# Optimization experiments

Measured on AMD Instinct MI355X. Metric: run time of the kernel, lower is better.

The kernel has to match this reference:

```python
import jax, jax.numpy as jnp
import numpy as np

IN_FEAT = 3 * 299 * 299  # 268203
D1 = 512
H = 28
OUT = 2


def setup_inputs() -> dict:
    key = jax.random.key(0)
    ks = jax.random.split(key, 10)
    B, T = 4, 64
    s1 = 1.0 / np.sqrt(IN_FEAT)
    s2 = 1.0 / np.sqrt(D1)
    s3 = 1.0 / np.sqrt(H)
    return {
        "x": jax.random.normal(ks[0], (B, T, 3, 299, 299), jnp.float32),
        "W1": jax.random.uniform(ks[1], (IN_FEAT, D1), jnp.float32, -s1, s1),
        "b1": jax.random.uniform(ks[2], (D1,), jnp.float32, -s1, s1),
        "Wi": jax.random.uniform(ks[3], (D1, H), jnp.float32, -s2, s2),
        "Wr": jax.random.uniform(ks[4], (H, H), jnp.float32, -s3, s3),
        "br": jax.random.uniform(ks[5], (H,), jnp.float32, -s3, s3),
        "A": jax.random.normal(ks[6], (H,), jnp.float32),
        "tau": 1.0 + jax.random.uniform(ks[7], (H,), jnp.float32),  # positive time constants
        "W2": jax.random.uniform(ks[8], (H, OUT), jnp.float32, -s3, s3),
        "b2": jax.random.uniform(ks[9], (OUT,), jnp.float32, -s3, s3),
    }


def reference(x, W1, b1, Wi, Wr, br, A, tau, W2, b2):
    B, T = x.shape[0], x.shape[1]
    xf = x.reshape(B, T, -1)                      # [B, T, 268203]
    h1 = jax.nn.relu(jnp.einsum('btf,fd->btd', xf, W1) + b1)  # [B, T, 512]
    u = jnp.einsum('btd,dh->bth', h1, Wi)         # precomputed input drive [B, T, H]
    dt = 1.0

    def step(h, u_t):
        # fused-Euler LTC cell: f gates both time-constant and attractor A
        ft = jax.nn.sigmoid(u_t + h @ Wr + br)
        h_new = (h + dt * ft * A) / (1.0 + dt * (1.0 / tau + ft))
        return h_new, h_new

    h0 = jnp.zeros((B, H), x.dtype)
    _, hs = jax.lax.scan(step, h0, jnp.swapaxes(u, 0, 1))  # [T, B, H]
    last = jax.nn.relu(hs[-1])                    # relu then take last step
    out = last @ W2 + b2                          # [B, 2]
    return jax.nn.sigmoid(out)
```

## Files before the change

### kernel.cpp

```cpp
#include <hip/hip_runtime.h>
#include <hip/hip_bf16.h>

#define KTOT   268203
#define MROWS  256
#define NCOLS  512
#define HDIM   28
#define NSTEPS 8382
#define FSTEP  8381
#define KREM   11
#define BN     256

typedef __attribute__((ext_vector_type(4))) float  f32x4;
typedef __attribute__((ext_vector_type(8))) __bf16 bf16x8;

#define AUX_NT 2

static __device__ inline bf16x8 pack8(const float* f) {
    union { bf16x8 v; __hip_bfloat16 h[8]; } u;
    #pragma unroll
    for (int j = 0; j < 8; ++j) u.h[j] = __float2bfloat16(f[j]);
    return u.v;
}
static __device__ inline unsigned short bfbits(float v) {
    __hip_bfloat16 h = __float2bfloat16(v);
    union { __hip_bfloat16 h; unsigned short u; } c; c.h = h; return c.u;
}

__global__ __launch_bounds__(512, 2) void gemm1_kernel(
    const float* __restrict__ x, const float* __restrict__ W1,
    __hip_bfloat16* __restrict__ part, int steps_per, int nks)
{
    __shared__ __align__(16) float Albuf[2][MROWS * 32];
    __shared__ __align__(16) float Bbuf[2][32 * BN];

    const int tid  = threadIdx.x;
    const int lane = tid & 63;
    const int w    = tid >> 6;
    const int wm   = w >> 1;
    const int wn   = w & 1;

    int bx, ks;
    {
        const int id = blockIdx.x;
        if ((nks & 7) == 0) {
            const int xcd = id & 7;
            const int m_  = id >> 3;
            bx = m_ & 1;
            ks = ((m_ >> 1) << 3) | xcd;
        } else {
            bx = id & 1;
            ks = id >> 1;
        }
    }
    const int bcol = bx * BN;

    const int dlt = lane >> 5;
    const int m   = lane & 31;
    const int rw7 = (2 * w + dlt) & 7;
    const int ag  = (m >> 2) ^ rw7;
    const size_t a_off = (size_t)(2 * w + dlt) * KTOT + ag * 4 + (m & 3);
    const size_t b_off = bcol + (size_t)(lane) * 4;

    f32x4 acc[4][8];
    #pragma unroll
    for (int i = 0; i < 4; ++i)
        #pragma unroll
        for (int j = 0; j < 8; ++j)
            acc[i][j] = (f32x4){0.f, 0.f, 0.f, 0.f};

    const int s0 = ks * steps_per;
    int s1 = s0 + steps_per;
    if (s1 > NSTEPS) s1 = NSTEPS;
    int s1f = (s1 < FSTEP) ? s1 : FSTEP;
    int nfull = s1f - s0;
    if (nfull < 0) nfull = 0;

    auto issue_step = [&](int s, int buf) {
        const float* ap = x + a_off + (size_t)s * 32;
        #pragma unroll
        for (int i = 0; i < 16; ++i) {
            const float* gp = ap + (size_t)i * 16 * KTOT;
            char* lp = (char*)&Albuf[buf][0] + (i * 8 + w) * 256;
            __builtin_amdgcn_global_load_lds(
                (const __attribute__((address_space(1))) unsigned int*)(const void*)gp,
                (__attribute__((address_space(3))) unsigned int*)(void*)lp, 4, 0, 0);
        }
        const float* bp = W1 + b_off + (size_t)s * 32 * NCOLS;
        #pragma unroll
        for (int i = 0; i < 4; ++i) {
            const float* gp = bp + (size_t)(i * 8 + w) * NCOLS;
            char* lp = (char*)&Bbuf[buf][0] + (i * 8 + w) * 1024;
            __builtin_amdgcn_global_load_lds(
                (const __attribute__((address_space(1))) unsigned int*)(const void*)gp,
                (__attribute__((address_space(3))) unsigned int*)(void*)lp, 16, 0, AUX_NT);
        }
    };

    auto compute = [&](int buf) {
        const int rc = lane & 15, ko = lane >> 4;
        bf16x8 bq[8];
        #pragma unroll
        for (int ni = 0; ni < 8; ++ni) {
            const int colL = wn * 128 + ni * 16 + rc;
            float bf[8];
            #pragma unroll
            for (int j = 0; j < 8; ++j)
                bf[j] = Bbuf[buf][(ko * 8 + j) * BN + colL];
            bq[ni] = pack8(bf);
        }
        const int soff = ((2 * ko) ^ (rc & 7)) * 16;
        #pragma unroll
        for (int mi = 0; mi < 4; ++mi) {
            const int ab = (wm * 64 + mi * 16 + rc) * 128;
            float afv[8];
            *(f32x4*)&afv[0] = *(const f32x4*)((const char*)&Albuf[buf][0] + ab + soff);
            *(f32x4*)&afv[4] = *(const f32x4*)((const char*)&Albuf[buf][0] + ab + (soff ^ 16));
            const bf16x8 af = pack8(afv);
            #pragma unroll
            for (int ni = 0; ni < 8; ++ni)
                acc[mi][ni] = __builtin_amdgcn_mfma_f32_16x16x32_bf16(
                    af, bq[ni], acc[mi][ni], 0, 0, 0);
        }
    };

    if (nfull > 0) {
        issue_step(s0, 0);
        for (int t = 0; t < nfull; ++t) {
            asm volatile("s_waitcnt vmcnt(0)" ::: "memory");
            __builtin_amdgcn_s_barrier();
            __builtin_amdgcn_sched_barrier(0);
            if (t + 1 < nfull) issue_step(s0 + t + 1, (t + 1) & 1);
            compute(t & 1);
        }
    }

    if (s1 > FSTEP && s0 < s1) {
        const int buf = nfull & 1;
        __syncthreads();
        {
            const int row = tid >> 1, half = tid & 1;
            #pragma unroll
            for (int i = 0; i < 16; ++i) {
                const int k = half * 16 + i;
                const float v = (k < KREM)
                    ? x[(size_t)row * KTOT + (size_t)FSTEP * 32 + k] : 0.f;
                Albuf[buf][row * 32 + ((k >> 2) ^ (row & 7)) * 4 + (k & 3)] = v;
            }
        }
        {
            const int c = tid & 255, og = tid >> 8;
            #pragma unroll
            for (int i = 0; i < 16; ++i) {
                const int k = og * 16 + i;
                const float v = (k < KREM)
                    ? W1[(size_t)(FSTEP * 32 + k) * NCOLS + bcol + c] : 0.f;
                Bbuf[buf][k * BN + c] = v;
            }
        }
        __syncthreads();
        compute(buf);
    }

    __hip_bfloat16* outp = part + (size_t)ks * MROWS * NCOLS;
    const int rc = lane & 15, q = lane >> 4;
    #pragma unroll
    for (int mi = 0; mi < 4; ++mi) {
        #pragma unroll
        for (int ni = 0; ni < 8; ++ni) {
            const int col = bcol + wn * 128 + ni * 16 + rc;
            #pragma unroll
            for (int j = 0; j < 4; ++j) {
                const int row = wm * 64 + mi * 16 + q * 4 + j;
                const float v  = acc[mi][ni][j];
                const float vh = __shfl_xor(v, 1);
                if (!(rc & 1)) {
                    const unsigned int pk =
                        (unsigned int)bfbits(v) | ((unsigned int)bfbits(vh) << 16);
                    *(unsigned int*)(outp + (size_t)row * NCOLS + col) = pk;
                }
            }
        }
    }
}

__global__ __launch_bounds__(512) void reduce_u_kernel(
    const __hip_bfloat16* __restrict__ part, const float* __restrict__ b1,
    const float* __restrict__ Wi, float* __restrict__ u, int nks)
{
    __shared__ float h1[NCOLS];
    __shared__ f32x4 red[4][128];
    const int row = blockIdx.x;
    const int tid = threadIdx.x;
    const int c4  = tid & 127;
    const int kk  = tid >> 7;

    const unsigned short* pu = (const unsigned short*)part;
    f32x4 sum = (f32x4){0.f, 0.f, 0.f, 0.f};
    for (int k = kk; k < nks; k += 4) {
        const size_t base = ((size_t)k * MROWS + row) * NCOLS + c4 * 4;
        ushort4 pv = *(const ushort4*)&pu[base];
        union { unsigned int u; float f; } c0, c1, c2, c3;
        c0.u = (unsigned int)pv.x << 16; c1.u = (unsigned int)pv.y << 16;
        c2.u = (unsigned int)pv.z << 16; c3.u = (unsigned int)pv.w << 16;
        sum[0] += c0.f; sum[1] += c1.f; sum[2] += c2.f; sum[3] += c3.f;
    }
    red[kk][c4] = sum;
    __syncthreads();

    if (tid < 128) {
        f32x4 t = red[0][tid] + red[1][tid] + red[2][tid] + red[3][tid];
        const f32x4 bb = *(const f32x4*)&b1[tid * 4];
        t += bb;
        #pragma unroll
        for (int j = 0; j < 4; ++j) h1[tid * 4 + j] = fmaxf(t[j], 0.f);
    }
    __syncthreads();

    const int wv = tid >> 6, lane = tid & 63;
    #pragma unroll
    for (int hh = 0; hh < 4; ++hh) {
        const int h = wv * 4 + hh;
        if (h < HDIM) {
            float p = 0.f;
            #pragma unroll
            for (int dd = 0; dd < 8; ++dd) {
                const int d = lane + dd * 64;
                p += h1[d] * Wi[d * HDIM + h];
            }
            #pragma unroll
            for (int off = 32; off; off >>= 1) p += __shfl_down(p, off);
            if (lane == 0) u[row * HDIM + h] = p;
        }
    }
}

__global__ __launch_bounds__(64) void recur_kernel(
    const float* __restrict__ u, const float* __restrict__ Wr,
    const float* __restrict__ br, const float* __restrict__ Av,
    const float* __restrict__ tau, const float* __restrict__ W2,
    const float* __restrict__ b2, float* __restrict__ out)
{
    const int b = blockIdx.x;
    const int j = threadIdx.x;
    const bool act = j < HDIM;
    const int jj = act ? j : 0;

    float wr[HDIM];
    #pragma unroll
    for (int i = 0; i < HDIM; ++i) wr[i] = act ? Wr[i * HDIM + jj] : 0.f;
    const float brj = act ? br[jj] : 0.f;
    const float Aj  = act ? Av[jj] : 0.f;
    const float itj = act ? (1.f / tau[jj]) : 0.f;

    float uv[64];
    #pragma unroll
    for (int t = 0; t < 64; ++t)
        uv[t] = act ? u[(b * 64 + t) * HDIM + jj] : 0.f;

    float h = 0.f;
    #pragma unroll
    for (int t = 0; t < 64; ++t) {
        float a = uv[t] + brj;
        #pragma unroll
        for (int i = 0; i < HDIM; ++i)
            a += __shfl(h, i) * wr[i];
        const float ft = 1.f / (1.f + expf(-a));
        const float hn = (h + ft * Aj) / (1.f + itj + ft);
        h = act ? hn : 0.f;
    }

    const float r  = act ? fmaxf(h, 0.f) : 0.f;
    float p0 = act ? r * W2[jj * 2 + 0] : 0.f;
    float p1 = act ? r * W2[jj * 2 + 1] : 0.f;
    #pragma unroll
    for (int off = 32; off; off >>= 1) {
        p0 += __shfl_down(p0, off);
        p1 += __shfl_down(p1, off);
    }
    if (j == 0) {
        out[b * 2 + 0] = 1.f / (1.f + expf(-(p0 + b2[0])));
        out[b * 2 + 1] = 1.f / (1.f + expf(-(p1 + b2[1])));
    }
}

extern "C" void kernel_launch(void* const* d_in, const int* in_sizes, int n_in,
                              void* d_out, int out_size, void* d_ws, size_t ws_size,
                              hipStream_t stream)
{
    (void)in_sizes; (void)n_in; (void)out_size;
    const float* x   = (const float*)d_in[0];
    const float* W1  = (const float*)d_in[1];
    const float* b1  = (const float*)d_in[2];
    const float* Wi  = (const float*)d_in[3];
    const float* Wr  = (const float*)d_in[4];
    const float* br  = (const float*)d_in[5];
    const float* Av  = (const float*)d_in[6];
    const float* tau = (const float*)d_in[7];
    const float* W2  = (const float*)d_in[8];
    const float* b2  = (const float*)d_in[9];
    float* out = (float*)d_out;

    const size_t per_split = (size_t)MROWS * NCOLS * sizeof(__hip_bfloat16);
    int nks = 128;
    while (nks > 8 && (size_t)nks * per_split + (1 << 16) > ws_size) nks >>= 1;
    const int steps_per = (NSTEPS + nks - 1) / nks;

    __hip_bfloat16* part = (__hip_bfloat16*)d_ws;
    float* u = (float*)((char*)d_ws + (size_t)nks * per_split);

    gemm1_kernel<<<dim3(2 * nks), 512, 0, stream>>>(x, W1, part, steps_per, nks);
    reduce_u_kernel<<<dim3(MROWS), 512, 0, stream>>>(part, b1, Wi, u, nks);
    recur_kernel<<<dim3(4), 64, 0, stream>>>(u, Wr, br, Av, tau, W2, b2, out);
}
```

Baseline: 282.3 us.

## Pre-convert x to swizzled bf16 and triple-buffer the split-K GEMM pipeline

Adds a prep kernel that converts x to bf16 in a pre-swizzled per-step layout. The GEMM can then fetch A tiles with 16-byte direct-to-LDS loads and read them as bf16 fragments, with no per-tile fp32-to-bf16 packing. The main loop moves from double to triple buffering with partial vmcnt waits, and the W1 tile in LDS gets an XOR swizzle. The cost is an extra kernel launch and more total memory traffic, since x is read once in fp32, written in bf16, then read twice, plus a larger LDS footprint.

```diff
diff --git a/kernel.cpp b/kernel.cpp
--- a/kernel.cpp
+++ b/kernel.cpp
@@ -10,8 +10,9 @@
 #define KREM   11
 #define BN     256
 
-typedef __attribute__((ext_vector_type(4))) float  f32x4;
-typedef __attribute__((ext_vector_type(8))) __bf16 bf16x8;
+typedef __attribute__((ext_vector_type(4))) float          f32x4;
+typedef __attribute__((ext_vector_type(8))) unsigned short u16x8;
+typedef __attribute__((ext_vector_type(8))) __bf16         bf16x8;
 
 #define AUX_NT 2
 
@@ -26,12 +27,35 @@
     union { __hip_bfloat16 h; unsigned short u; } c; c.h = h; return c.u;
 }
 
+__global__ __launch_bounds__(512) void xprep_kernel(
+    const float* __restrict__ x, __hip_bfloat16* __restrict__ xb)
+{
+    const size_t g = (size_t)blockIdx.x * 512 + threadIdx.x;
+    const int s   = (int)(g >> 10);
+    const int j   = (int)(g & 1023);
+    const int row = j >> 2;
+    const int t   = j & 3;
+    const int oct = t ^ ((row >> 1) & 3);
+    const long k0 = (long)s * 32 + oct * 8;
+    const float* src = x + (size_t)row * KTOT + k0;
+    union { u16x8 v; unsigned short u[8]; } o;
+    if (s < FSTEP) {
+        #pragma unroll
+        for (int e = 0; e < 8; ++e) o.u[e] = bfbits(src[e]);
+    } else {
+        #pragma unroll
+        for (int e = 0; e < 8; ++e)
+            o.u[e] = (k0 + e < KTOT) ? bfbits(src[e]) : (unsigned short)0;
+    }
+    *(u16x8*)((unsigned short*)xb + g * 8) = o.v;
+}
+
 __global__ __launch_bounds__(512, 2) void gemm1_kernel(
-    const float* __restrict__ x, const float* __restrict__ W1,
+    const __hip_bfloat16* __restrict__ xb, const float* __restrict__ W1,
     __hip_bfloat16* __restrict__ part, int steps_per, int nks)
 {
-    __shared__ __align__(16) float Albuf[2][MROWS * 32];
-    __shared__ __align__(16) float Bbuf[2][32 * BN];
+    __shared__ __align__(16) __hip_bfloat16 Albuf[3][MROWS * 32];
+    __shared__ __align__(16) float          Bbuf[3][32 * BN];
 
     const int tid  = threadIdx.x;
     const int lane = tid & 63;
@@ -54,13 +78,6 @@
     }
     const int bcol = bx * BN;
 
-    const int dlt = lane >> 5;
-    const int m   = lane & 31;
-    const int rw7 = (2 * w + dlt) & 7;
-    const int ag  = (m >> 2) ^ rw7;
-    const size_t a_off = (size_t)(2 * w + dlt) * KTOT + ag * 4 + (m & 3);
-    const size_t b_off = bcol + (size_t)(lane) * 4;
-
     f32x4 acc[4][8];
     #pragma unroll
     for (int i = 0; i < 4; ++i)
@@ -75,21 +92,24 @@
     int nfull = s1f - s0;
     if (nfull < 0) nfull = 0;
 
-    auto issue_step = [&](int s, int buf) {
-        const float* ap = x + a_off + (size_t)s * 32;
-        #pragma unroll
-        for (int i = 0; i < 16; ++i) {
-            const float* gp = ap + (size_t)i * 16 * KTOT;
-            char* lp = (char*)&Albuf[buf][0] + (i * 8 + w) * 256;
+    auto issueA = [&](int s, int buf) {
+        const unsigned short* base = (const unsigned short*)xb + (size_t)s * 8192;
+        #pragma unroll
+        for (int i = 0; i < 2; ++i) {
+            const unsigned short* gp = base + (size_t)(i * 512 + tid) * 8;
+            char* lp = (char*)&Albuf[buf][0] + (i * 512 + w * 64) * 16;
             __builtin_amdgcn_global_load_lds(
                 (const __attribute__((address_space(1))) unsigned int*)(const void*)gp,
-                (__attribute__((address_space(3))) unsigned int*)(void*)lp, 4, 0, 0);
-        }
-        const float* bp = W1 + b_off + (size_t)s * 32 * NCOLS;
+                (__attribute__((address_space(3))) unsigned int*)(void*)lp, 16, 0, 0);
+        }
+    };
+    auto issueB = [&](int s, int buf) {
         #pragma unroll
         for (int i = 0; i < 4; ++i) {
-            const float* gp = bp + (size_t)(i * 8 + w) * NCOLS;
-            char* lp = (char*)&Bbuf[buf][0] + (i * 8 + w) * 1024;
+            const int krow = i * 8 + w;
+            const float* gp = W1 + ((size_t)s * 32 + krow) * NCOLS + bcol
+                                 + ((4 * lane) ^ (8 * i));
+            char* lp = (char*)&Bbuf[buf][0] + (i * 512 + w * 64) * 16;
             __builtin_amdgcn_global_load_lds(
                 (const __attribute__((address_space(1))) unsigned int*)(const void*)gp,
                 (__attribute__((address_space(3))) unsigned int*)(void*)lp, 16, 0, AUX_NT);
@@ -102,20 +122,18 @@
         #pragma unroll
         for (int ni = 0; ni < 8; ++ni) {
             const int colL = wn * 128 + ni * 16 + rc;
+            const int slot = colL ^ (8 * ko);
             float bf[8];
             #pragma unroll
             for (int j = 0; j < 8; ++j)
-                bf[j] = Bbuf[buf][(ko * 8 + j) * BN + colL];
+                bf[j] = Bbuf[buf][(ko * 8 + j) * BN + slot];
             bq[ni] = pack8(bf);
         }
-        const int soff = ((2 * ko) ^ (rc & 7)) * 16;
+        const int tslot = ko ^ ((rc >> 1) & 3);
         #pragma unroll
         for (int mi = 0; mi < 4; ++mi) {
-            const int ab = (wm * 64 + mi * 16 + rc) * 128;
-            float afv[8];
-            *(f32x4*)&afv[0] = *(const f32x4*)((const char*)&Albuf[buf][0] + ab + soff);
-            *(f32x4*)&afv[4] = *(const f32x4*)((const char*)&Albuf[buf][0] + ab + (soff ^ 16));
-            const bf16x8 af = pack8(afv);
+            const int row = wm * 64 + mi * 16 + rc;
+            const bf16x8 af = *(const bf16x8*)&Albuf[buf][(row * 4 + tslot) * 8];
             #pragma unroll
             for (int ni = 0; ni < 8; ++ni)
                 acc[mi][ni] = __builtin_amdgcn_mfma_f32_16x16x32_bf16(
@@ -124,29 +142,29 @@
     };
 
     if (nfull > 0) {
-        issue_step(s0, 0);
+        issueA(s0, 0); issueB(s0, 0);
+        if (nfull > 1) { issueA(s0 + 1, 1); issueB(s0 + 1, 1); }
+        int buf = 0;
         for (int t = 0; t < nfull; ++t) {
-            asm volatile("s_waitcnt vmcnt(0)" ::: "memory");
+            if (t + 1 < nfull) { asm volatile("s_waitcnt vmcnt(6)" ::: "memory"); }
+            else               { asm volatile("s_waitcnt vmcnt(0)" ::: "memory"); }
+            __builtin_amdgcn_sched_barrier(0);
             __builtin_amdgcn_s_barrier();
             __builtin_amdgcn_sched_barrier(0);
-            if (t + 1 < nfull) issue_step(s0 + t + 1, (t + 1) & 1);
-            compute(t & 1);
+            if (t + 2 < nfull) {
+                const int nb2 = (buf >= 1) ? buf - 1 : 2;
+                issueA(s0 + t + 2, nb2); issueB(s0 + t + 2, nb2);
+                __builtin_amdgcn_sched_barrier(0);
+            }
+            compute(buf);
+            __builtin_amdgcn_sched_barrier(0);
+            buf = (buf == 2) ? 0 : buf + 1;
         }
     }
 
     if (s1 > FSTEP && s0 < s1) {
-        const int buf = nfull & 1;
-        __syncthreads();
-        {
-            const int row = tid >> 1, half = tid & 1;
-            #pragma unroll
-            for (int i = 0; i < 16; ++i) {
-                const int k = half * 16 + i;
-                const float v = (k < KREM)
-                    ? x[(size_t)row * KTOT + (size_t)FSTEP * 32 + k] : 0.f;
-                Albuf[buf][row * 32 + ((k >> 2) ^ (row & 7)) * 4 + (k & 3)] = v;
-            }
-        }
+        const int buf = nfull % 3;
+        issueA(FSTEP, buf);
         {
             const int c = tid & 255, og = tid >> 8;
             #pragma unroll
@@ -154,7 +172,7 @@
                 const int k = og * 16 + i;
                 const float v = (k < KREM)
                     ? W1[(size_t)(FSTEP * 32 + k) * NCOLS + bcol + c] : 0.f;
-                Bbuf[buf][k * BN + c] = v;
+                Bbuf[buf][k * BN + (c ^ (8 * (k >> 3)))] = v;
             }
         }
         __syncthreads();
@@ -300,15 +318,19 @@
     const float* b2  = (const float*)d_in[9];
     float* out = (float*)d_out;
 
+    const size_t xb_bytes = (size_t)NSTEPS * 1024 * 16;
+    __hip_bfloat16* xbuf = (__hip_bfloat16*)d_ws;
+
     const size_t per_split = (size_t)MROWS * NCOLS * sizeof(__hip_bfloat16);
     int nks = 128;
-    while (nks > 8 && (size_t)nks * per_split + (1 << 16) > ws_size) nks >>= 1;
+    while (nks > 8 && xb_bytes + (size_t)nks * per_split + (1 << 16) > ws_size) nks >>= 1;
     const int steps_per = (NSTEPS + nks - 1) / nks;
 
-    __hip_bfloat16* part = (__hip_bfloat16*)d_ws;
-    float* u = (float*)((char*)d_ws + (size_t)nks * per_split);
-
-    gemm1_kernel<<<dim3(2 * nks), 512, 0, stream>>>(x, W1, part, steps_per, nks);
+    __hip_bfloat16* part = (__hip_bfloat16*)((char*)d_ws + xb_bytes);
+    float* u = (float*)((char*)part + (size_t)nks * per_split);
+
+    xprep_kernel<<<dim3(NSTEPS * 2), 512, 0, stream>>>(x, xbuf);
+    gemm1_kernel<<<dim3(2 * nks), 512, 0, stream>>>(xbuf, W1, part, steps_per, nks);
     reduce_u_kernel<<<dim3(MROWS), 512, 0, stream>>>(part, b1, Wi, u, nks);
     recur_kernel<<<dim3(4), 64, 0, stream>>>(u, Wr, br, Av, tau, W2, b2, out);
 }
```

New measurement: 322.0 us. +14.1%, slower.
